# Performance work log

Hardware: AMD Instinct MI355X
Metric: run time of the kernel (lower is better)

Reference implementation:

```python
import jax, jax.numpy as jnp
import numpy as np

DIM = 1024
IMG_H, IMG_W = 512, 1408
CROP = 224
IMAGE_ORDER = (2, 0, 1, 5, 3, 4)
B, NC, NB = 2, 6, 32


def setup_inputs():
    key = jax.random.key(0)
    ks = jax.random.split(key, 12)
    camera_imgs = jax.random.normal(ks[0], (B, NC, 3, IMG_H, IMG_W), jnp.float32)
    u = jax.random.uniform(ks[1], (B, NB, 9), dtype=jnp.float32)
    centers = jnp.stack([u[..., 0] * 45.0 + 5.0,
                         (u[..., 1] - 0.5) * 40.0,
                         (u[..., 2] - 0.5) * 4.0], -1)
    pred_boxes = jnp.concatenate([centers, u[..., 3:] * 2.0], -1)  # [B,NB,9]
    K = np.array([[500., 0., IMG_W / 2.], [0., 500., IMG_H / 2.], [0., 0., 1.]])
    R_l2c = np.array([[0., -1., 0.], [0., 0., -1.], [1., 0., 0.]])  # lidar->camera axes
    mats = np.zeros((NC, 4, 4), np.float32)
    for c in range(NC):
        yaw = 2.0 * np.pi * c / NC
        Rz = np.array([[np.cos(yaw), -np.sin(yaw), 0.], [np.sin(yaw), np.cos(yaw), 0.], [0., 0., 1.]])
        mats[c, :3, :3] = K @ R_l2c @ Rz.T
        mats[c, 3, 3] = 1.0
    lidar2image = jnp.broadcast_to(jnp.asarray(mats), (B, NC, 4, 4))
    eye4 = jnp.eye(4, dtype=jnp.float32)
    img_aug_matrix = jnp.broadcast_to(eye4, (B, NC, 4, 4))
    lidar_aug_matrix = jnp.broadcast_to(eye4, (B, 4, 4))
    momentum = jnp.float32(0.5)
    box_default_dim = jax.random.normal(ks[2], (1, DIM), jnp.float32)
    theta_w = jnp.zeros((4, 9), jnp.float32)  # zero-init as in torch code
    theta_b = jnp.array([1., 0., 0., 1.], jnp.float32)

    def cw(k, shape):
        fan = shape[1] * shape[2] * shape[3]
        return jax.random.normal(k, shape, jnp.float32) * (2.0 / fan) ** 0.5
    conv1 = cw(ks[3], (64, 3, 7, 7))
    conv2 = cw(ks[4], (256, 64, 3, 3))
    conv3 = cw(ks[5], (DIM, 256, 3, 3))
    pos_embed = jax.random.normal(ks[6], (50, DIM), jnp.float32) * 0.02
    s = DIM ** -0.5
    wq = jax.random.normal(ks[7], (DIM, DIM), jnp.float32) * s
    wk = jax.random.normal(ks[8], (DIM, DIM), jnp.float32) * s
    wv = jax.random.normal(ks[9], (DIM, DIM), jnp.float32) * s
    wo = jax.random.normal(ks[10], (DIM, DIM), jnp.float32) * s
    return dict(camera_imgs=camera_imgs, pred_boxes=pred_boxes,
                img_aug_matrix=img_aug_matrix, lidar_aug_matrix=lidar_aug_matrix,
                lidar2image=lidar2image, momentum=momentum,
                box_default_dim=box_default_dim, theta_w=theta_w, theta_b=theta_b,
                conv1=conv1, conv2=conv2, conv3=conv3, pos_embed=pos_embed,
                wq=wq, wk=wk, wv=wv, wo=wo)


def _project(pred_boxes, lidar_aug_matrix, lidar2image, img_aug_matrix):
    # returns vu [B,NC,NB,2] = (row, col) pixel coords, on_img [B,NC,NB]
    def per_b(boxes, la, l2i, aug):
        c = boxes[:, :3] - la[:3, 3]                       # [NB,3]
        c = jnp.linalg.inv(la[:3, :3]) @ c.T               # [3,NB]
        c = l2i[:, :3, :3] @ c + l2i[:, :3, 3:4]           # [NC,3,NB]
        z = jnp.clip(c[:, 2], 1e-5, 1e5)
        xy = c[:, :2] / z[:, None]
        c = jnp.concatenate([xy, z[:, None]], 1)
        c = aug[:, :3, :3] @ c + aug[:, :3, 3:4]
        uv = c[:, :2].transpose(0, 2, 1)                   # [NC,NB,2] (col,row)
        vu = uv[..., ::-1]                                 # (row,col)
        on = (vu[..., 0] < IMG_H) & (vu[..., 0] >= 0) & (vu[..., 1] < IMG_W) & (vu[..., 1] >= 0)
        return vu, on
    return jax.vmap(per_b)(pred_boxes, lidar_aug_matrix, lidar2image, img_aug_matrix)


def _base_grid(h, w):
    # torch affine_grid align_corners=False pixel-center coords
    xs = (2.0 * jnp.arange(w) + 1.0) / w - 1.0
    ys = (2.0 * jnp.arange(h) + 1.0) / h - 1.0
    gx, gy = jnp.meshgrid(xs, ys)  # [h,w]
    return jnp.stack([gx, gy, jnp.ones_like(gx)], -1)  # [h,w,3]


def _grid_sample(img, grid):
    # img [C,H,W]; grid [...,2] xy in [-1,1]; bilinear, zeros padding, align_corners=False
    C, H, W = img.shape
    ix = ((grid[..., 0] + 1.0) * W - 1.0) / 2.0
    iy = ((grid[..., 1] + 1.0) * H - 1.0) / 2.0
    x0 = jnp.floor(ix); y0 = jnp.floor(iy)
    x1 = x0 + 1.0; y1 = y0 + 1.0
    wx = ix - x0; wy = iy - y0

    def gather(xx, yy):
        xi = jnp.clip(xx, 0, W - 1).astype(jnp.int32)
        yi = jnp.clip(yy, 0, H - 1).astype(jnp.int32)
        valid = (xx >= 0) & (xx <= W - 1) & (yy >= 0) & (yy <= H - 1)
        return img[:, yi, xi] * valid.astype(img.dtype)  # [C, ...]
    v00 = gather(x0, y0); v01 = gather(x1, y0)
    v10 = gather(x0, y1); v11 = gather(x1, y1)
    return (v00 * (1 - wx) * (1 - wy) + v01 * wx * (1 - wy)
            + v10 * (1 - wx) * wy + v11 * wx * wy)  # [C, ...]


def _clip_head(x, conv1, conv2, conv3, pos_embed, wq, wk, wv, wo):
    dn = ('NCHW', 'OIHW', 'NCHW')
    h = jax.nn.relu(jax.lax.conv_general_dilated(x, conv1, (4, 4), 'SAME', dimension_numbers=dn))
    h = jax.nn.relu(jax.lax.conv_general_dilated(h, conv2, (4, 4), 'SAME', dimension_numbers=dn))
    h = jax.nn.relu(jax.lax.conv_general_dilated(h, conv3, (2, 2), 'SAME', dimension_numbers=dn))  # [M,D,7,7]
    tok = h.reshape(h.shape[0], DIM, 49).transpose(0, 2, 1)              # [M,49,D]
    tok = jnp.concatenate([tok.mean(1, keepdims=True), tok], 1) + pos_embed  # [M,50,D]
    q = tok[:, :1] @ wq
    k = tok @ wk
    v = tok @ wv
    attn = jax.nn.softmax((q @ k.transpose(0, 2, 1)) * (DIM ** -0.5), -1)
    return ((attn @ v) @ wo)[:, 0]  # [M,D]


def reference(camera_imgs, pred_boxes, img_aug_matrix, lidar_aug_matrix, lidar2image,
              momentum, box_default_dim, theta_w, theta_b,
              conv1, conv2, conv3, pos_embed, wq, wk, wv, wo):
    N = B * NB
    vu, on_img = _project(pred_boxes, lidar_aug_matrix, lidar2image, img_aug_matrix)  # [B,NC,NB,2],[B,NC,NB]
    boxes_flat = pred_boxes.reshape(N, 9)
    rot = jnp.tanh(boxes_flat @ theta_w.T + theta_b).reshape(N, 2, 2)   # theta_rot MLP
    ty = vu[..., 0] / IMG_H * 2.0 - 1.0                                 # [B,NC,NB]
    tx = vu[..., 1] / IMG_W * 2.0 - 1.0
    pos = jnp.stack([tx, ty], -1).transpose(0, 2, 1, 3).reshape(N, NC, 2)
    theta = jnp.concatenate([jnp.broadcast_to(rot[:, None], (N, NC, 2, 2)),
                             pos[..., None]], -1)                        # [N,NC,2,3]
    base = _base_grid(CROP, CROP)                                        # [224,224,3]
    grids = jnp.einsum('hwk,ncjk->nchwj', base, theta)                   # [N,NC,224,224,2]
    grids = grids.reshape(B, NB, NC, CROP, CROP, 2)
    crops = []
    for b in range(B):
        for c in range(NC):
            smp = _grid_sample(camera_imgs[b, c], grids[b, :, c])        # [3,NB,224,224]
            crops.append(smp.transpose(1, 0, 2, 3))
    crops = jnp.stack(crops).reshape(B, NC, NB, 3, CROP, CROP)
    crops = crops.transpose(0, 2, 1, 3, 4, 5).reshape(N * NC, 3, CROP, CROP)
    emb = _clip_head(crops, conv1, conv2, conv3, pos_embed, wq, wk, wv, wo).reshape(N, NC, DIM)
    valid = on_img.transpose(0, 2, 1).reshape(N, NC)
    e = jnp.broadcast_to(box_default_dim, (N, DIM))
    for c in IMAGE_ORDER:  # sequential EMA over cameras, skipping off-image ones
        m = valid[:, c:c + 1]
        e = jnp.where(m, momentum * e + (1.0 - momentum) * emb[:, c], e)
    return e  # [N, DIM]
```

## Files before the change

### kernel.cpp

```cpp
#include <hip/hip_runtime.h>
#include <hip/hip_bf16.h>

#define DIMN 1024
#define IMG_H 512
#define IMG_W 1408
#define CROPN 224
#define NCAM 6
#define NBOXB 32
#define NBOX 64
#define NIMG 384

typedef __hip_bfloat16 bf16;
typedef unsigned short u16;
typedef float f32x4 __attribute__((ext_vector_type(4)));
typedef short bf16x8 __attribute__((ext_vector_type(8)));
typedef u16 u16x4 __attribute__((ext_vector_type(4)));
typedef u16 u16x8 __attribute__((ext_vector_type(8)));

__device__ __forceinline__ float b2f(bf16 x) { return __bfloat162float(x); }
__device__ __forceinline__ u16 f2us(float x) {
  bf16 h = __float2bfloat16(x);
  return *(u16*)&h;
}
__device__ __forceinline__ bf16x8 as_b(u16x8 x) {
  union { u16x8 u; bf16x8 b; } c; c.u = x; return c.b;
}

__global__ void k_w1r(const float* __restrict__ in, u16* __restrict__ out) {
  int idx = blockIdx.x * 256 + threadIdx.x;
  if (idx >= 64 * 224) return;
  int oc = idx / 224, t = idx % 224;
  int r = t >> 5, u = t & 31, kw = u >> 2, ch = u & 3;
  u16 v = (kw < 7 && ch < 3) ? f2us(in[((oc * 3 + ch) * 7 + r) * 7 + kw]) : (u16)0;
  out[(((oc >> 4) * 28 + (t >> 3)) * 16 + (oc & 15)) * 8 + (t & 7)] = v;
}
__global__ void k_w2r(const float* __restrict__ in, u16* __restrict__ out) {
  int idx = blockIdx.x * 256 + threadIdx.x;
  if (idx >= 256 * 576) return;
  int oc = idx / 576, t = idx % 576;
  int rk = t >> 6, ic = t & 63, r = rk / 3, kw = rk % 3;
  out[idx] = f2us(in[((oc * 64 + ic) * 3 + r) * 3 + kw]);
}
__global__ void k_w3r(const float* __restrict__ in, u16* __restrict__ out) {
  int idx = blockIdx.x * 256 + threadIdx.x;
  if (idx >= 1024 * 2304) return;
  int oc = idx / 2304, t = idx % 2304;
  int rk = t >> 8, ic = t & 255, r = rk / 3, kw = rk % 3;
  u16 v = f2us(in[((oc * 256 + ic) * 3 + r) * 3 + kw]);
  int ocb = oc >> 4, mm = oc & 15, kb = t >> 3, kj = t & 7;
  out[(((size_t)ocb * 288 + kb) * 16 + mm) * 8 + kj] = v;
}
__global__ void k_transpose_t(const float* __restrict__ w, float* __restrict__ wt) {
  __shared__ float tile[32][33];
  int x = blockIdx.x * 32 + threadIdx.x;
  for (int j = threadIdx.y; j < 32; j += 8)
    tile[j][threadIdx.x] = w[(size_t)(blockIdx.y * 32 + j) * 1024 + x];
  __syncthreads();
  int x2 = blockIdx.y * 32 + threadIdx.x;
  for (int j = threadIdx.y; j < 32; j += 8)
    wt[(size_t)(blockIdx.x * 32 + j) * 1024 + x2] = tile[threadIdx.x][j];
}

__global__ void k_proj(const float* __restrict__ boxes, const float* __restrict__ la_m,
                       const float* __restrict__ l2i, const float* __restrict__ aug,
                       const float* __restrict__ tw, const float* __restrict__ tb,
                       float* __restrict__ theta_out, int* __restrict__ valid_out) {
  int t = threadIdx.x;
  if (t >= NIMG) return;
  int n = t / NCAM, cam = t % NCAM;
  int b = n / NBOXB, nb = n % NBOXB;

  float la[4][4];
  for (int r = 0; r < 4; r++)
    for (int c = 0; c < 4; c++) la[r][c] = la_m[b * 16 + r * 4 + c];
  float a00=la[0][0],a01=la[0][1],a02=la[0][2];
  float a10=la[1][0],a11=la[1][1],a12=la[1][2];
  float a20=la[2][0],a21=la[2][1],a22=la[2][2];
  float c00 =  a11*a22 - a12*a21;
  float c01 = -(a10*a22 - a12*a20);
  float c02 =  a10*a21 - a11*a20;
  float det = a00*c00 + a01*c01 + a02*c02;
  float id = 1.0f / det;
  float inv[3][3];
  inv[0][0] = c00*id;                 inv[0][1] = -(a01*a22-a02*a21)*id;  inv[0][2] =  (a01*a12-a02*a11)*id;
  inv[1][0] = c01*id;                 inv[1][1] =  (a00*a22-a02*a20)*id;  inv[1][2] = -(a00*a12-a02*a10)*id;
  inv[2][0] = c02*id;                 inv[2][1] = -(a00*a21-a01*a20)*id;  inv[2][2] =  (a00*a11-a01*a10)*id;

  float bx[9];
  for (int i = 0; i < 9; i++) bx[i] = boxes[(b * NBOXB + nb) * 9 + i];
  float c0[3] = { bx[0]-la[0][3], bx[1]-la[1][3], bx[2]-la[2][3] };
  float c1[3];
  for (int r = 0; r < 3; r++) c1[r] = inv[r][0]*c0[0] + inv[r][1]*c0[1] + inv[r][2]*c0[2];

  const float* M = l2i + (size_t)(b * NCAM + cam) * 16;
  float p[3];
  for (int r = 0; r < 3; r++)
    p[r] = M[r*4+0]*c1[0] + M[r*4+1]*c1[1] + M[r*4+2]*c1[2] + M[r*4+3];
  float z = fminf(fmaxf(p[2], 1e-5f), 100000.0f);
  float x = p[0] / z, y = p[1] / z;
  const float* A = aug + (size_t)(b * NCAM + cam) * 16;
  float u = A[0]*x + A[1]*y + A[2]*z + A[3];
  float v = A[4]*x + A[5]*y + A[6]*z + A[7];

  int on = (v < (float)IMG_H) && (v >= 0.0f) && (u < (float)IMG_W) && (u >= 0.0f);
  float ty = v / (float)IMG_H * 2.0f - 1.0f;
  float tx = u / (float)IMG_W * 2.0f - 1.0f;

  float s[4];
  for (int j = 0; j < 4; j++) {
    float acc = tb[j];
    for (int i = 0; i < 9; i++) acc += tw[j * 9 + i] * bx[i];
    s[j] = tanhf(acc);
  }
  float* o = theta_out + t * 6;
  o[0] = s[0]; o[1] = s[1]; o[2] = tx;
  o[3] = s[2]; o[4] = s[3]; o[5] = ty;
  valid_out[t] = on;
}

#define HALO_PX 1356
__global__ void k_zero_halo(u16x4* __restrict__ c) {
  int t = blockIdx.x * 256 + threadIdx.x;
  int i = t / HALO_PX;
  if (i >= NIMG) return;
  int r = t % HALO_PX;
  int ph, pw;
  if (r < 684) {
    int rr = r / 228;
    ph = (rr == 0) ? 0 : (rr == 1 ? 225 : 226);
    pw = r % 228;
  } else {
    int q = r - 684;
    ph = 1 + q / 3;
    int s = q % 3;
    pw = (s == 0) ? 0 : (s == 1 ? 225 : 226);
  }
  c[(size_t)i * 228 * 228 + ph * 228 + pw] = (u16x4){0, 0, 0, 0};
}

__global__ __launch_bounds__(256) void k_sample(const float* __restrict__ imgs,
                                                const float* __restrict__ theta,
                                                u16* __restrict__ crops) {
  int idx = blockIdx.x * 256 + threadIdx.x;
  int i = idx / (CROPN * CROPN);
  int rem = idx - i * (CROPN * CROPN);
  int yy = rem / CROPN, xx = rem % CROPN;
  const float* th = theta + i * 6;
  float gx = (2.0f * xx + 1.0f) / (float)CROPN - 1.0f;
  float gy = (2.0f * yy + 1.0f) / (float)CROPN - 1.0f;
  float grid_x = th[0]*gx + th[1]*gy + th[2];
  float grid_y = th[3]*gx + th[4]*gy + th[5];
  float ix = ((grid_x + 1.0f) * (float)IMG_W - 1.0f) * 0.5f;
  float iy = ((grid_y + 1.0f) * (float)IMG_H - 1.0f) * 0.5f;
  float x0 = floorf(ix), y0 = floorf(iy);
  float wx = ix - x0, wy = iy - y0;
  int cam = i % NCAM, b = i / (NBOXB * NCAM);
  const float* base = imgs + (size_t)(b * NCAM + cam) * 3 * IMG_H * IMG_W;

  float xf[2] = { x0, x0 + 1.0f };
  float yf[2] = { y0, y0 + 1.0f };
  float wxa[2] = { 1.0f - wx, wx };
  float wya[2] = { 1.0f - wy, wy };
  int   xi[2], yi[2], vx[2], vy[2];
  for (int j = 0; j < 2; j++) {
    vx[j] = (xf[j] >= 0.0f) && (xf[j] <= (float)(IMG_W - 1));
    vy[j] = (yf[j] >= 0.0f) && (yf[j] <= (float)(IMG_H - 1));
    xi[j] = (int)fminf(fmaxf(xf[j], 0.0f), (float)(IMG_W - 1));
    yi[j] = (int)fminf(fmaxf(yf[j], 0.0f), (float)(IMG_H - 1));
  }
  float res[3];
  #pragma unroll
  for (int ch = 0; ch < 3; ch++) {
    const float* cp = base + (size_t)ch * IMG_H * IMG_W;
    float r = 0.0f;
    #pragma unroll
    for (int jy = 0; jy < 2; jy++)
      #pragma unroll
      for (int jx = 0; jx < 2; jx++) {
        float val = (vx[jx] && vy[jy]) ? cp[yi[jy] * IMG_W + xi[jx]] : 0.0f;
        r += val * wxa[jx] * wya[jy];
      }
    res[ch] = r;
  }
  u16x4 st = { f2us(res[0]), f2us(res[1]), f2us(res[2]), 0 };
  *(u16x4*)(crops + ((size_t)i * 228 * 228 + (size_t)(yy + 1) * 228 + (xx + 1)) * 4) = st;
}


#define C1_GROUPS 34
__global__ __launch_bounds__(256) void k_conv1m(const u16* __restrict__ X,
                                                const u16* __restrict__ W,
                                                u16* __restrict__ out) {
  __shared__ u16x8 sX[C1_GROUPS * 64];
  int blk = blockIdx.x;
  int i = blk / 14, rg = blk % 14;
  int tid = threadIdx.x, wv = tid >> 6, lane = tid & 63;
  int m = lane & 15, quad = lane >> 4;

  const u16* src = X + ((size_t)i * 51984 + (size_t)(rg * 16) * 228) * 4;
  #pragma unroll
  for (int j = 0; j < 9; j++) {
    int g = wv + j * 4;
    if (g < C1_GROUPS) {
      int c = g * 64 + lane;
      int cc = c < 2166 ? c : 2165;
      __builtin_amdgcn_global_load_lds(
          (const __attribute__((address_space(1))) void*)(src + (size_t)cc * 8),
          (__attribute__((address_space(3))) void*)(sX + g * 64),
          16, 0, 0);
    }
  }
  __syncthreads();

  int col[4];
  #pragma unroll
  for (int nt = 0; nt < 4; nt++) col[nt] = nt * 16 + m;
  f32x4 acc[4][4];
  #pragma unroll
  for (int t = 0; t < 4; t++)
    #pragma unroll
    for (int nt = 0; nt < 4; nt++) acc[t][nt] = (f32x4){0.f, 0.f, 0.f, 0.f};

  #pragma unroll
  for (int r = 0; r < 7; r++) {
    bf16x8 a[4];
    #pragma unroll
    for (int t = 0; t < 4; t++)
      a[t] = as_b(*(const u16x8*)(W + (size_t)(((t * 28 + r * 4 + quad) * 16 + m) * 8)));
    int lrow = wv * 4 + r;
    #pragma unroll
    for (int nt = 0; nt < 4; nt++) {
      int cl = col[nt] < 56 ? col[nt] : 55;
      bf16x8 bfr = as_b(sX[lrow * 114 + cl * 2 + quad]);
      #pragma unroll
      for (int t = 0; t < 4; t++)
        acc[t][nt] = __builtin_amdgcn_mfma_f32_16x16x32_bf16(a[t], bfr, acc[t][nt], 0, 0, 0);
    }
  }
  int oh = rg * 4 + wv;
  #pragma unroll
  for (int nt = 0; nt < 4; nt++) {
    if (col[nt] < 56) {
      int n = oh * 56 + col[nt];
      #pragma unroll
      for (int t = 0; t < 4; t++) {
        u16x4 st;
        #pragma unroll
        for (int r4 = 0; r4 < 4; r4++) st[r4] = f2us(fmaxf(acc[t][nt][r4], 0.f));
        *(u16x4*)(out + ((size_t)i * 3136 + n) * 64 + t * 16 + quad * 4) = st;
      }
    }
  }
}

__global__ __launch_bounds__(256) void k_conv2m(const u16* __restrict__ X,
                                                const u16* __restrict__ W,
                                                u16* __restrict__ out) {
  int blk = blockIdx.x;
  int i = blk >> 2, og = blk & 3;
  int oc0 = og * 64;
  int tid = threadIdx.x, wv = tid >> 6, lane = tid & 63;
  int m = lane & 15, quad = lane >> 4;
  int narr[4];
  const u16* bp[4];
  #pragma unroll
  for (int nt = 0; nt < 4; nt++) {
    int n = wv * 64 + nt * 16 + m;
    narr[nt] = n;
    int nc = n < 196 ? n : 195;
    int oh = nc / 14, ow = nc - oh * 14;
    bp[nt] = X + ((size_t)i * 3136 + (size_t)(oh * 4) * 56 + ow * 4) * 64 + quad * 8;
  }
  f32x4 acc[4][4];
  #pragma unroll
  for (int t = 0; t < 4; t++)
    #pragma unroll
    for (int nt = 0; nt < 4; nt++) acc[t][nt] = (f32x4){0.f, 0.f, 0.f, 0.f};

  #pragma unroll
  for (int s = 0; s < 18; s++) {
    const int rk = s >> 1, r = rk / 3, kw = rk % 3;
    const int boff = ((r * 56 + kw) * 64 + (s & 1) * 32);
    bf16x8 a[4];
    #pragma unroll
    for (int t = 0; t < 4; t++)
      a[t] = as_b(*(const u16x8*)(W + (size_t)(oc0 + t * 16 + m) * 576 + s * 32 + quad * 8));
    #pragma unroll
    for (int nt = 0; nt < 4; nt++) {
      bf16x8 bfr = as_b(*(const u16x8*)(bp[nt] + boff));
      #pragma unroll
      for (int t = 0; t < 4; t++)
        acc[t][nt] = __builtin_amdgcn_mfma_f32_16x16x32_bf16(a[t], bfr, acc[t][nt], 0, 0, 0);
    }
  }
  #pragma unroll
  for (int nt = 0; nt < 4; nt++) {
    int n = narr[nt];
    if (n < 196) {
      #pragma unroll
      for (int t = 0; t < 4; t++) {
        u16x4 st;
        #pragma unroll
        for (int r4 = 0; r4 < 4; r4++) st[r4] = f2us(fmaxf(acc[t][nt][r4], 0.f));
        *(u16x4*)(out + ((size_t)i * 196 + n) * 256 + oc0 + t * 16 + quad * 4) = st;
      }
    }
  }
}

__global__ __launch_bounds__(512, 2) void k_conv3m(const u16* __restrict__ X,
                                                   const u16* __restrict__ W,
                                                   float* __restrict__ out3) {
  __shared__ u16x8 sX8[6688];
  int bid = blockIdx.x;
  int og = (bid >> 2) & 1;
  int i  = (bid >> 3) * 4 + (bid & 3);
  int tid = threadIdx.x;

  const u16* src = X + (size_t)i * (196 * 256);
  u16x8 tmp[13];
  #pragma unroll
  for (int j = 0; j < 13; j++) {
    int c = tid + j * 512;
    int cc = c < 6272 ? c : 6271;
    tmp[j] = *(const u16x8*)(src + (size_t)cc * 8);
  }
  #pragma unroll
  for (int j = 0; j < 13; j++) {
    int c = tid + j * 512;
    sX8[(c & ~31) | ((c & 31) ^ ((c >> 6) & 7))] = tmp[j];
  }
  if (tid < 32) sX8[6656 + tid] = (u16x8){0,0,0,0,0,0,0,0};
  __syncthreads();

  int wv = tid >> 6, lane = tid & 63;
  int m = lane & 15, quad = lane >> 4;
  int ocw = og * 512 + wv * 64;
  int narr[4], oh2[4], ow2[4];
  #pragma unroll
  for (int nt = 0; nt < 4; nt++) {
    int n = nt * 16 + m;
    narr[nt] = n;
    int nc = n < 49 ? n : 48;
    int oh = nc / 7, ow = nc - oh * 7;
    oh2[nt] = oh * 2; ow2[nt] = ow * 2;
  }
  f32x4 acc[4][4];
  #pragma unroll
  for (int t = 0; t < 4; t++)
    #pragma unroll
    for (int nt = 0; nt < 4; nt++) acc[t][nt] = (f32x4){0.f, 0.f, 0.f, 0.f};

  const u16* wbase = W + (size_t)(ocw >> 4) * (288 * 128) + m * 8;

  #pragma unroll
  for (int rk = 0; rk < 9; rk++) {
    const int r = rk / 3, kw = rk % 3;
    int bck[4], bxr[4];
    #pragma unroll
    for (int nt = 0; nt < 4; nt++) {
      int ih = oh2[nt] + r, iw = ow2[nt] + kw;
      bool valid = (narr[nt] < 49) && (ih < 14) && (iw < 14);
      int p = ih * 14 + iw;
      bck[nt] = valid ? p * 32 : 6656;
      bxr[nt] = valid ? ((p >> 1) & 7) : 0;
    }
    #pragma unroll
    for (int ic8 = 0; ic8 < 8; ic8++) {
      const int kblk = rk * 32 + ic8 * 4 + quad;
      bf16x8 a[4];
      #pragma unroll
      for (int t = 0; t < 4; t++)
        a[t] = as_b(*(const u16x8*)(wbase + ((size_t)t * 288 + kblk) * 128));
      const int q = ic8 * 4 + quad;
      #pragma unroll
      for (int nt = 0; nt < 4; nt++) {
        bf16x8 bfr = as_b(sX8[bck[nt] + (q ^ bxr[nt])]);
        #pragma unroll
        for (int t = 0; t < 4; t++)
          acc[t][nt] = __builtin_amdgcn_mfma_f32_16x16x32_bf16(a[t], bfr, acc[t][nt], 0, 0, 0);
      }
    }
  }
  #pragma unroll
  for (int nt = 0; nt < 4; nt++) {
    int n = narr[nt];
    if (n < 49) {
      #pragma unroll
      for (int t = 0; t < 4; t++) {
        f32x4 o;
        #pragma unroll
        for (int r4 = 0; r4 < 4; r4++) o[r4] = fmaxf(acc[t][nt][r4], 0.f);
        *(f32x4*)(out3 + ((size_t)i * 49 + n) * DIMN + ocw + t * 16 + quad * 4) = o;
      }
    }
  }
}

__global__ __launch_bounds__(256) void k_tok(const float* __restrict__ h,
                                             const float* __restrict__ pos,
                                             float* __restrict__ tok) {
  int blk = blockIdx.x;
  int i = blk / 50, t = blk % 50;
  int d = threadIdx.x * 4;
  float4 val;
  if (t == 0) {
    float sx = 0, sy = 0, sz = 0, sw = 0;
    for (int p = 0; p < 49; p++) {
      float4 v = *(const float4*)(h + ((size_t)i * 49 + p) * DIMN + d);
      sx += v.x; sy += v.y; sz += v.z; sw += v.w;
    }
    const float inv49 = 1.0f / 49.0f;
    val.x = sx * inv49; val.y = sy * inv49; val.z = sz * inv49; val.w = sw * inv49;
  } else {
    val = *(const float4*)(h + ((size_t)i * 49 + (t - 1)) * DIMN + d);
  }
  float4 pe = *(const float4*)(pos + (size_t)t * DIMN + d);
  float4 o; o.x = val.x + pe.x; o.y = val.y + pe.y; o.z = val.z + pe.z; o.w = val.w + pe.w;
  *(float4*)(tok + ((size_t)i * 50 + t) * DIMN + d) = o;
}

__global__ __launch_bounds__(256) void k_matvec2(const float* __restrict__ vecs, int vstride,
                                                 const float* __restrict__ M,
                                                 float* __restrict__ out) {
  __shared__ float s_v[4][DIMN];
  int i0 = blockIdx.x * 4;
  int h = blockIdx.y;
  for (int e = threadIdx.x; e < 4 * DIMN; e += 256)
    s_v[e >> 10][e & 1023] = vecs[(size_t)(i0 + (e >> 10)) * vstride + (e & 1023)];
  __syncthreads();
  int d0 = h * 512 + threadIdx.x * 2;
  float2 acc[4] = {{0,0},{0,0},{0,0},{0,0}};
  for (int e = 0; e < DIMN; e++) {
    float2 w = *(const float2*)(M + (size_t)e * DIMN + d0);
    #pragma unroll
    for (int im = 0; im < 4; im++) {
      float x = s_v[im][e];
      acc[im].x += x * w.x; acc[im].y += x * w.y;
    }
  }
  #pragma unroll
  for (int im = 0; im < 4; im++)
    *(float2*)(out + (size_t)(i0 + im) * DIMN + d0) = acc[im];
}

__global__ __launch_bounds__(256) void k_attn(const float* __restrict__ tok,
                                              const float* __restrict__ a1,
                                              float* __restrict__ tvec) {
  __shared__ float s_a[DIMN];
  __shared__ float s_sc[50];
  __shared__ float s_at[50];
  int i = blockIdx.x;
  for (int e = threadIdx.x; e < DIMN; e += 256) s_a[e] = a1[(size_t)i * DIMN + e];
  __syncthreads();
  int wave = threadIdx.x >> 6, lane = threadIdx.x & 63;
  for (int t = wave; t < 50; t += 4) {
    const float* tr = tok + ((size_t)i * 50 + t) * DIMN;
    float p = 0.0f;
    for (int mm = 0; mm < 16; mm++) {
      int e = lane + mm * 64;
      p += tr[e] * s_a[e];
    }
    for (int off = 32; off > 0; off >>= 1) p += __shfl_down(p, off, 64);
    if (lane == 0) s_sc[t] = p * 0.03125f;
  }
  __syncthreads();
  if (threadIdx.x == 0) {
    float mx = s_sc[0];
    for (int t = 1; t < 50; t++) mx = fmaxf(mx, s_sc[t]);
    float sum = 0.0f;
    for (int t = 0; t < 50; t++) { float ex = expf(s_sc[t] - mx); s_at[t] = ex; sum += ex; }
    float inv = 1.0f / sum;
    for (int t = 0; t < 50; t++) s_at[t] *= inv;
  }
  __syncthreads();
  int d0 = threadIdx.x * 4;
  float ax = 0, ay = 0, az = 0, aw = 0;
  for (int t = 0; t < 50; t++) {
    float at = s_at[t];
    float4 tv = *(const float4*)(tok + ((size_t)i * 50 + t) * DIMN + d0);
    ax += at * tv.x; ay += at * tv.y; az += at * tv.z; aw += at * tv.w;
  }
  float4 o; o.x = ax; o.y = ay; o.z = az; o.w = aw;
  *(float4*)(tvec + (size_t)i * DIMN + d0) = o;
}

__global__ void k_final(const float* __restrict__ emb,
                        const int* __restrict__ valid,
                        const float* __restrict__ bdd,
                        const float* __restrict__ momp,
                        float* __restrict__ out) {
  int n = blockIdx.x;
  int d0 = threadIdx.x * 4;
  float mom = momp[0];
  float e[4];
  #pragma unroll
  for (int j = 0; j < 4; j++) e[j] = bdd[d0 + j];
  const int order[6] = {2, 0, 1, 5, 3, 4};
  #pragma unroll
  for (int s = 0; s < 6; s++) {
    int c = order[s];
    int i = n * NCAM + c;
    if (valid[i]) {
      const float* er = emb + (size_t)i * DIMN + d0;
      #pragma unroll
      for (int j = 0; j < 4; j++) e[j] = mom * e[j] + (1.0f - mom) * er[j];
    }
  }
  #pragma unroll
  for (int j = 0; j < 4; j++) out[(size_t)n * DIMN + d0 + j] = e[j];
}

extern "C" void kernel_launch(void* const* d_in, const int* in_sizes, int n_in,
                              void* d_out, int out_size, void* d_ws, size_t ws_size,
                              hipStream_t stream) {
  const float* in_cam = (const float*)d_in[0];
  const float* in_box = (const float*)d_in[1];
  const float* in_aug = (const float*)d_in[2];
  const float* in_la  = (const float*)d_in[3];
  const float* in_l2i = (const float*)d_in[4];
  const float* in_mom = (const float*)d_in[5];
  const float* in_bdd = (const float*)d_in[6];
  const float* in_tw  = (const float*)d_in[7];
  const float* in_tb  = (const float*)d_in[8];
  const float* in_c1  = (const float*)d_in[9];
  const float* in_c2  = (const float*)d_in[10];
  const float* in_c3  = (const float*)d_in[11];
  const float* in_pe  = (const float*)d_in[12];
  const float* in_wq  = (const float*)d_in[13];
  const float* in_wk  = (const float*)d_in[14];
  const float* in_wv  = (const float*)d_in[15];
  const float* in_wo  = (const float*)d_in[16];

  char* base = (char*)d_ws;
  size_t off = 0;
  auto carve = [&](size_t bytes) -> char* {
    char* p = base + off;
    off += (bytes + 255) & ~(size_t)255;
    return p;
  };
  float* theta   = (float*)carve((size_t)NIMG * 6 * 4);
  int*   valid   = (int*)carve((size_t)NIMG * 4);
  float* qbuf    = (float*)carve((size_t)NIMG * DIMN * 4);
  float* a1buf   = (float*)carve((size_t)NIMG * DIMN * 4);
  float* tvbuf   = (float*)carve((size_t)NIMG * DIMN * 4);
  float* ctxbuf  = (float*)carve((size_t)NIMG * DIMN * 4);
  float* embbuf  = (float*)carve((size_t)NIMG * DIMN * 4);
  float* wkT_f   = (float*)carve((size_t)DIMN * DIMN * 4);
  u16*   W1r     = (u16*)carve((size_t)64 * 224 * 2);
  u16*   W2r     = (u16*)carve((size_t)256 * 576 * 2);
  u16*   W3r     = (u16*)carve((size_t)1024 * 2304 * 2);
  u16*   c2o     = (u16*)carve((size_t)NIMG * 196 * 256 * 2);
  char*  R1      = carve((size_t)NIMG * 228 * 228 * 4 * 2);
  u16*   c1o     = (u16*)carve((size_t)NIMG * 3136 * 64 * 2);
  u16*   crops   = (u16*)R1;
  float* conv3o  = (float*)R1;
  float* tok     = (float*)(R1 + (size_t)NIMG * 49 * DIMN * 4);

  k_w1r<<<56, 256, 0, stream>>>(in_c1, W1r);
  k_w2r<<<576, 256, 0, stream>>>(in_c2, W2r);
  k_w3r<<<9216, 256, 0, stream>>>(in_c3, W3r);
  k_transpose_t<<<dim3(32, 32), dim3(32, 8), 0, stream>>>(in_wk, wkT_f);

  k_proj<<<1, 384, 0, stream>>>(in_box, in_la, in_l2i, in_aug, in_tw, in_tb, theta, valid);
  k_zero_halo<<<(NIMG * HALO_PX + 255) / 256, 256, 0, stream>>>((u16x4*)crops);
  k_sample<<<(NIMG * CROPN * CROPN) / 256, 256, 0, stream>>>(in_cam, theta, crops);
  k_conv1m<<<NIMG * 14, 256, 0, stream>>>(crops, W1r, c1o);
  k_conv2m<<<NIMG * 4, 256, 0, stream>>>(c1o, W2r, c2o);
  k_conv3m<<<768, 512, 0, stream>>>(c2o, W3r, conv3o);
  k_tok<<<NIMG * 50, 256, 0, stream>>>(conv3o, in_pe, tok);
  k_matvec2<<<dim3(96, 2), 256, 0, stream>>>(tok, 50 * DIMN, in_wq, qbuf);
  k_matvec2<<<dim3(96, 2), 256, 0, stream>>>(qbuf, DIMN, wkT_f, a1buf);
  k_attn<<<NIMG, 256, 0, stream>>>(tok, a1buf, tvbuf);
  k_matvec2<<<dim3(96, 2), 256, 0, stream>>>(tvbuf, DIMN, in_wv, ctxbuf);
  k_matvec2<<<dim3(96, 2), 256, 0, stream>>>(ctxbuf, DIMN, in_wo, embbuf);
  k_final<<<NBOX, 256, 0, stream>>>(embbuf, valid, in_bdd, in_mom, (float*)d_out);
}
```

Baseline: 1.009 ms.

## Software-pipeline conv3 MFMA loads and change LDS swizzle to avoid bank conflicts

The conv3 implicit-GEMM loop is flattened into 72 k-steps. Global weight fragments are prefetched two steps ahead in a triple buffer and LDS activation fragments one step ahead in a double buffer, so memory latency overlaps the MFMAs. The LDS XOR swizzle now uses ((iw>>1)-(ih>>1))&7, derived from spatial coordinates, to cut bank conflicts for the stride-2 access pattern. Keeping more fragments in flight raises register pressure and may lower occupancy.

```diff
diff --git a/kernel.cpp b/kernel.cpp
--- a/kernel.cpp
+++ b/kernel.cpp
@@ -328,7 +328,10 @@
   #pragma unroll
   for (int j = 0; j < 13; j++) {
     int c = tid + j * 512;
-    sX8[(c & ~31) | ((c & 31) ^ ((c >> 6) & 7))] = tmp[j];
+    int p = c >> 5, kc = c & 31;
+    int ih = p / 14, iw = p - ih * 14;
+    int gsw = ((iw >> 1) - (ih >> 1)) & 7;
+    sX8[(c & ~31) | (kc ^ gsw)] = tmp[j];
   }
   if (tid < 32) sX8[6656 + tid] = (u16x8){0,0,0,0,0,0,0,0};
   __syncthreads();
@@ -353,35 +356,53 @@
 
   const u16* wbase = W + (size_t)(ocw >> 4) * (288 * 128) + m * 8;
 
-  #pragma unroll
-  for (int rk = 0; rk < 9; rk++) {
+  int bc[4], bk[4];
+  auto set_bparams = [&](int rk) {
     const int r = rk / 3, kw = rk % 3;
-    int bck[4], bxr[4];
     #pragma unroll
     for (int nt = 0; nt < 4; nt++) {
       int ih = oh2[nt] + r, iw = ow2[nt] + kw;
       bool valid = (narr[nt] < 49) && (ih < 14) && (iw < 14);
       int p = ih * 14 + iw;
-      bck[nt] = valid ? p * 32 : 6656;
-      bxr[nt] = valid ? ((p >> 1) & 7) : 0;
-    }
-    #pragma unroll
-    for (int ic8 = 0; ic8 < 8; ic8++) {
-      const int kblk = rk * 32 + ic8 * 4 + quad;
-      bf16x8 a[4];
+      bc[nt] = valid ? p * 32 : 6656;
+      bk[nt] = valid ? (((iw >> 1) - (ih >> 1)) & 7) : 0;
+    }
+  };
+  auto loadA = [&](int t, int s) {
+    return as_b(*(const u16x8*)(wbase + (size_t)(t * 288 + 4 * s + quad) * 128));
+  };
+  auto loadB = [&](int nt, int q4) {
+    return as_b(sX8[bc[nt] + ((q4 + quad) ^ bk[nt])]);
+  };
+
+  bf16x8 A_[3][4], B_[2][4];
+  set_bparams(0);
+  #pragma unroll
+  for (int t = 0; t < 4; t++) {
+    A_[0][t] = loadA(t, 0);
+    A_[1][t] = loadA(t, 1);
+  }
+  #pragma unroll
+  for (int nt = 0; nt < 4; nt++) B_[0][nt] = loadB(nt, 0);
+
+  #pragma unroll
+  for (int s = 0; s < 72; s++) {
+    if (s + 2 < 72) {
+      #pragma unroll
+      for (int t = 0; t < 4; t++) A_[(s + 2) % 3][t] = loadA(t, s + 2);
+    }
+    if (s + 1 < 72) {
+      if (((s + 1) & 7) == 0) set_bparams((s + 1) >> 3);
+      #pragma unroll
+      for (int nt = 0; nt < 4; nt++) B_[(s + 1) & 1][nt] = loadB(nt, ((s + 1) & 7) * 4);
+    }
+    #pragma unroll
+    for (int nt = 0; nt < 4; nt++)
       #pragma unroll
       for (int t = 0; t < 4; t++)
-        a[t] = as_b(*(const u16x8*)(wbase + ((size_t)t * 288 + kblk) * 128));
-      const int q = ic8 * 4 + quad;
-      #pragma unroll
-      for (int nt = 0; nt < 4; nt++) {
-        bf16x8 bfr = as_b(sX8[bck[nt] + (q ^ bxr[nt])]);
-        #pragma unroll
-        for (int t = 0; t < 4; t++)
-          acc[t][nt] = __builtin_amdgcn_mfma_f32_16x16x32_bf16(a[t], bfr, acc[t][nt], 0, 0, 0);
-      }
-    }
-  }
+        acc[t][nt] = __builtin_amdgcn_mfma_f32_16x16x32_bf16(A_[s % 3][t], B_[s & 1][nt], acc[t][nt], 0, 0, 0);
+  }
+
   #pragma unroll
   for (int nt = 0; nt < 4; nt++) {
     int n = narr[nt];
```

Result: faster. 986.0 us (-2.3%).
